# Optimization experiments

Measured on AMD Instinct MI355X. Metric: run time of the kernel, lower is better.

The kernel has to match this reference:

```python
import jax, jax.numpy as jnp
import numpy as np


def setup_inputs() -> dict:
    key = jax.random.key(0)
    ks = jax.random.split(key, 8)
    B, S, H, I = 2, 1025, 3200, 12800
    T = B * S
    # int8 tensors represented as int32, symmetric range [-128, 126]
    hidden_states = jax.random.randint(ks[0], (B, S, H), 0, 255, dtype=jnp.int32) - 127
    scale_in = (jax.random.uniform(ks[1], (T,)) * 0.02 + 1e-4).astype(jnp.float16)
    w1 = jax.random.randint(ks[2], (I, H), 0, 255, dtype=jnp.int32) - 127
    w1_scale = (jax.random.uniform(ks[3], (I,)) * 0.01 + 1e-4).astype(jnp.float32)
    b1 = (jax.random.normal(ks[4], (I,)) * 0.02).astype(jnp.float16)
    w2 = jax.random.randint(ks[5], (H, I), 0, 255, dtype=jnp.int32) - 127
    w2_scale = (jax.random.uniform(ks[6], (H,)) * 0.01 + 1e-4).astype(jnp.float32)
    b2 = (jax.random.normal(ks[7], (H,)) * 0.02).astype(jnp.float16)
    return {"hidden_states": hidden_states, "scale_in": scale_in,
            "w1": w1, "w1_scale": w1_scale, "b1": b1,
            "w2": w2, "w2_scale": w2_scale, "b2": b2}


def _w8a8_linear(x_int, scale_x, w_int, w_scale, bias):
    # int8 GEMM with int32 accumulation, dequant with per-token * per-channel scales
    acc = jnp.matmul(x_int, w_int.T)  # [T, out] int32
    out = acc.astype(jnp.float32) * scale_x[:, None].astype(jnp.float32) * w_scale[None, :]
    return (out + bias.astype(jnp.float32)).astype(jnp.float16)


def _gelu_and_quant(x_f16):
    # fused GELU + per-token dynamic symmetric int8 quantization
    g = jax.nn.gelu(x_f16.astype(jnp.float32), approximate=False)  # [T, I]
    amax = jnp.max(jnp.abs(g), axis=-1)                              # [T]
    scale_act = (amax / 127.0).astype(jnp.float16)
    s = jnp.maximum(scale_act.astype(jnp.float32), 1e-8)
    q = jnp.clip(jnp.round(g / s[:, None]), -128, 127).astype(jnp.int32)
    return q, scale_act


def reference(hidden_states, scale_in, w1, w1_scale, b1, w2, w2_scale, b2):
    B, S, H = hidden_states.shape
    x = hidden_states.reshape(-1, H)               # [T, H] int
    fc1_out = _w8a8_linear(x, scale_in, w1, w1_scale, b1)      # [T, I] fp16
    act_out, scale_act = _gelu_and_quant(fc1_out)              # int8-as-int32, [T] fp16
    fc2_out = _w8a8_linear(act_out, scale_act, w2, w2_scale, b2)  # [T, H] fp16
    return fc2_out
```

## Files before the change

### kernel.cpp

```cpp
#include <hip/hip_runtime.h>
#include <hip/hip_fp16.h>

typedef int v4i __attribute__((ext_vector_type(4)));

#define AS1C(p) ((const __attribute__((address_space(1))) void*)(p))
#define AS3(p)  ((__attribute__((address_space(3))) void*)(p))

__global__ void pack1(const int* __restrict__ a, const int* __restrict__ b,
                      signed char* __restrict__ pa, signed char* __restrict__ pb,
                      unsigned int* __restrict__ amax,
                      long long na, long long nb, int T) {
  const long long gid = blockIdx.x * (long long)blockDim.x + threadIdx.x;
  if (gid < T) amax[gid] = 0u;
  const long long n4a = na >> 2, n4b = nb >> 2;
  const long long tot = n4a + n4b;
  const long long stride = (long long)gridDim.x * blockDim.x;
  for (long long u = gid; u < tot; u += stride) {
    const int* src; signed char* dst; long long loc;
    if (u < n4a) { src = a; dst = pa; loc = u; }
    else         { src = b; dst = pb; loc = u - n4a; }
    const int4 v = *(const int4*)(src + (loc << 2));
    const unsigned out = (unsigned)(v.x & 0xff) | ((unsigned)(v.y & 0xff) << 8) |
                         ((unsigned)(v.z & 0xff) << 16) | ((unsigned)(v.w & 0xff) << 24);
    *(unsigned*)(dst + (loc << 2)) = out;
  }
}

__launch_bounds__(1024, 4)
__global__ void fc1_fused(const signed char* __restrict__ A, const signed char* __restrict__ Bw,
                          int M, int N, int K,
                          const float* __restrict__ scale_tok, const float* __restrict__ wsc,
                          const float* __restrict__ bias,
                          __half* __restrict__ gout, unsigned int* __restrict__ amax,
                          const int* __restrict__ w2src, signed char* __restrict__ w2dst,
                          long long n4w2, int npack, int gy) {
  __shared__ __align__(16) char smem[2][32768];
  const int bid = blockIdx.x;

  if (bid < npack) {
    const long long stride = (long long)npack * 1024;
    for (long long u = (long long)bid * 1024 + threadIdx.x; u < n4w2; u += stride) {
      const int4 v = *(const int4*)(w2src + (u << 2));
      const unsigned out = (unsigned)(v.x & 0xff) | ((unsigned)(v.y & 0xff) << 8) |
                           ((unsigned)(v.z & 0xff) << 16) | ((unsigned)(v.w & 0xff) << 24);
      *(unsigned*)(w2dst + (u << 2)) = out;
    }
    return;
  }

  const int tid = threadIdx.x;
  const int lane = tid & 63, wave = tid >> 6;
  const int wavem = wave >> 2, waven = wave & 3;
  const int lh = lane & 15, sseg = lane >> 4;

  int lid;
  {
    const int o = bid - npack;
    const int nwg = gridDim.x - npack;
    const int q = nwg >> 3, r = nwg & 7;
    const int x = o & 7, p = o >> 3;
    lid = (x < r ? x * (q + 1) : r * (q + 1) + (x - r) * q) + p;
  }
  const long long t0 = (long long)(lid % gy) * 256;
  const long long n0 = (long long)(lid / gy) * 256;
  const int nk = K >> 6;
  const long long Mm1 = M - 1, Nm1 = N - 1;

  const int lr4 = lane >> 2, slot = lane & 3;
  const int rloc = wave * 16 + lr4;
  const int gslot = (slot ^ ((rloc >> 1) & 3)) << 4;
  const signed char* sp0;
  const signed char* sp1;
  {
    long long gr = t0 + rloc; if (gr > Mm1) gr = Mm1;
    sp0 = A + gr * (long long)K + gslot;
    long long gn = n0 + rloc; if (gn > Nm1) gn = Nm1;
    sp1 = Bw + gn * (long long)K + gslot;
  }
  const int d0 = wave * 1024, d1 = 16384 + wave * 1024;

#define STAGE(bi) do { \
    __builtin_amdgcn_global_load_lds(AS1C(sp0), AS3(&smem[bi][d0]), 16, 0, 0); sp0 += 64; \
    __builtin_amdgcn_global_load_lds(AS1C(sp1), AS3(&smem[bi][d1]), 16, 0, 0); sp1 += 64; \
  } while (0)

  const int xs = ((sseg ^ ((lh >> 1) & 3)) << 4);
  const int offA = wavem * 4096 + lh * 64 + xs;
  const int offB = 16384 + waven * 4096 + lh * 64 + xs;

  v4i acc[4][4] = {};

  STAGE(0);
  __syncthreads();

  int cur = 0;
  for (int kt = 0; kt < nk; ++kt) {
    if (kt + 1 < nk) STAGE(cur ^ 1);
    const char* base = smem[cur];
    v4i af[4], bf[2];
#pragma unroll
    for (int mi = 0; mi < 4; ++mi) af[mi] = *(const v4i*)(base + offA + mi * 1024);
    bf[0] = *(const v4i*)(base + offB);
    bf[1] = *(const v4i*)(base + offB + 1024);
#pragma unroll
    for (int mi = 0; mi < 4; ++mi) {
      acc[mi][0] = __builtin_amdgcn_mfma_i32_16x16x64_i8(af[mi], bf[0], acc[mi][0], 0, 0, 0);
      acc[mi][1] = __builtin_amdgcn_mfma_i32_16x16x64_i8(af[mi], bf[1], acc[mi][1], 0, 0, 0);
    }
    bf[0] = *(const v4i*)(base + offB + 2048);
    bf[1] = *(const v4i*)(base + offB + 3072);
#pragma unroll
    for (int mi = 0; mi < 4; ++mi) {
      acc[mi][2] = __builtin_amdgcn_mfma_i32_16x16x64_i8(af[mi], bf[0], acc[mi][2], 0, 0, 0);
      acc[mi][3] = __builtin_amdgcn_mfma_i32_16x16x64_i8(af[mi], bf[1], acc[mi][3], 0, 0, 0);
    }
    __syncthreads();
    cur ^= 1;
  }
#undef STAGE

  long long cidx[4]; float w4[4], bi4[4]; bool cok[4];
#pragma unroll
  for (int ni = 0; ni < 4; ++ni) {
    cidx[ni] = n0 + waven * 64 + ni * 16 + lh;
    cok[ni] = cidx[ni] < N;
    w4[ni] = cok[ni] ? wsc[cidx[ni]] : 0.f;
    bi4[ni] = cok[ni] ? bias[cidx[ni]] : 0.f;
  }
#pragma unroll
  for (int mi = 0; mi < 4; ++mi) {
#pragma unroll
    for (int j = 0; j < 4; ++j) {
      const long long t = t0 + wavem * 64 + mi * 16 + (lane >> 4) * 4 + j;
      const bool valid = t < M;
      const float st = valid ? scale_tok[t] : 0.f;
      float rowmax = 0.f;
#pragma unroll
      for (int ni = 0; ni < 4; ++ni) {
        float v = (float)acc[mi][ni][j] * st * w4[ni] + bi4[ni];
        v = __half2float(__float2half(v));
        const float gl = 0.5f * v * (1.f + erff(v * 0.70710678118654752f));
        rowmax = fmaxf(rowmax, fabsf(gl));
        if (valid && cok[ni]) gout[t * (long long)N + cidx[ni]] = __float2half(gl);
      }
#pragma unroll
      for (int m = 1; m < 16; m <<= 1) rowmax = fmaxf(rowmax, __shfl_xor(rowmax, m));
      if (valid && lh == 0) atomicMax(&amax[t], __float_as_uint(rowmax));
    }
  }
}

__device__ __forceinline__ void stage_tile(const signed char* __restrict__ g, long long ld,
                                           long long rmax, long long r0, int k0,
                                           char* lds, int tid) {
  const int wave = tid >> 6, lane = tid & 63;
#pragma unroll
  for (int p = 0; p < 2; ++p) {
    const int chunk = wave * 2 + p;
    const int row = chunk * 16 + (lane >> 2);
    const int slot = lane & 3;
    const int gslot = slot ^ ((row >> 1) & 3);
    long long rg = r0 + row;
    if (rg > rmax) rg = rmax;
    const signed char* src = g + rg * ld + (long long)k0 + gslot * 16;
    char* dst = lds + chunk * 1024;
    __builtin_amdgcn_global_load_lds(AS1C(src), AS3(dst), 16, 0, 0);
  }
}

__launch_bounds__(256, 4)
__global__ void gemm_fc2(const signed char* __restrict__ A, const signed char* __restrict__ Bw,
                         int M, int N, int K,
                         const float* __restrict__ wsc, const float* __restrict__ bias,
                         unsigned int* __restrict__ amax, float* __restrict__ fout) {
  __shared__ __align__(16) char lds[2][2][128 * 64];
  const int tid = threadIdx.x;
  const int lane = tid & 63, wave = tid >> 6;
  const int wrow = (wave >> 1) * 64, wcol = (wave & 1) * 64;

  const int gy = gridDim.y;
  int lid;
  {
    const int o = blockIdx.y * gridDim.x + blockIdx.x;
    const int nwg = gridDim.x * gy;
    const int q = nwg >> 3, r = nwg & 7;
    const int x = o & 7, p = o >> 3;
    lid = (x < r ? x * (q + 1) : r * (q + 1) + (x - r) * q) + p;
  }
  const long long t0 = (long long)(lid % gy) * 128;
  const long long n0 = (long long)(lid / gy) * 128;

  v4i acc[4][4] = {};

  stage_tile(A, K, (long long)M - 1, t0, 0, lds[0][0], tid);
  stage_tile(Bw, K, (long long)N - 1, n0, 0, lds[0][1], tid);
  __syncthreads();

  const int nk = K >> 6;
  int cur = 0;
  const int srow = lane & 15, sseg = lane >> 4;
  for (int kt = 0; kt < nk; ++kt) {
    if (kt + 1 < nk) {
      stage_tile(A, K, (long long)M - 1, t0, (kt + 1) << 6, lds[cur ^ 1][0], tid);
      stage_tile(Bw, K, (long long)N - 1, n0, (kt + 1) << 6, lds[cur ^ 1][1], tid);
    }
    v4i af[4], bf[4];
#pragma unroll
    for (int mi = 0; mi < 4; ++mi) {
      const int r = wrow + mi * 16 + srow;
      const int sl = sseg ^ ((r >> 1) & 3);
      af[mi] = *(const v4i*)&lds[cur][0][r * 64 + sl * 16];
    }
#pragma unroll
    for (int ni = 0; ni < 4; ++ni) {
      const int r = wcol + ni * 16 + srow;
      const int sl = sseg ^ ((r >> 1) & 3);
      bf[ni] = *(const v4i*)&lds[cur][1][r * 64 + sl * 16];
    }
#pragma unroll
    for (int mi = 0; mi < 4; ++mi)
#pragma unroll
      for (int ni = 0; ni < 4; ++ni)
        acc[mi][ni] = __builtin_amdgcn_mfma_i32_16x16x64_i8(af[mi], bf[ni], acc[mi][ni], 0, 0, 0);
    __syncthreads();
    cur ^= 1;
  }

#pragma unroll
  for (int mi = 0; mi < 4; ++mi) {
#pragma unroll
    for (int j = 0; j < 4; ++j) {
      const long long t = t0 + wrow + mi * 16 + (lane >> 4) * 4 + j;
      if (t < M) {
        const float am = __uint_as_float(amax[t]);
        const float st = __half2float(__float2half(am * (1.f / 127.f)));
#pragma unroll
        for (int ni = 0; ni < 4; ++ni) {
          const long long c = n0 + wcol + ni * 16 + (lane & 15);
          const float v = (float)acc[mi][ni][j] * st * wsc[c] + bias[c];
          fout[t * (long long)N + c] = __half2float(__float2half(v));
        }
      }
    }
  }
}

__global__ void gelu_quant(const __half* __restrict__ g, const unsigned int* __restrict__ amax,
                           signed char* __restrict__ q, long long total, int I) {
  const long long nchunk = total >> 3;
  const long long stride = (long long)gridDim.x * blockDim.x;
  for (long long c = blockIdx.x * (long long)blockDim.x + threadIdx.x; c < nchunk; c += stride) {
    const long long base = c << 3;
    const int t = (int)(base / I);
    const float am = __uint_as_float(amax[t]);
    const float s = fmaxf(__half2float(__float2half(am * (1.f / 127.f))), 1e-8f);
    const float inv = 1.f / s;
    const int4 raw = *(const int4*)(g + base);
    const __half2* h2 = (const __half2*)&raw;
    union { signed char b[8]; int2 v; } u;
#pragma unroll
    for (int k = 0; k < 4; ++k) {
      const float2 f = __half22float2(h2[k]);
      const float q0 = fminf(fmaxf(rintf(f.x * inv), -128.f), 127.f);
      const float q1 = fminf(fmaxf(rintf(f.y * inv), -128.f), 127.f);
      u.b[k * 2]     = (signed char)(int)q0;
      u.b[k * 2 + 1] = (signed char)(int)q1;
    }
    *(int2*)(q + base) = u.v;
  }
}

extern "C" void kernel_launch(void* const* d_in, const int* in_sizes, int n_in,
                              void* d_out, int out_size, void* d_ws, size_t ws_size,
                              hipStream_t stream) {
  const int* hs = (const int*)d_in[0];
  const float* scale_in = (const float*)d_in[1];
  const int* w1 = (const int*)d_in[2];
  const float* w1s = (const float*)d_in[3];
  const float* b1 = (const float*)d_in[4];
  const int* w2 = (const int*)d_in[5];
  const float* w2s = (const float*)d_in[6];
  const float* b2 = (const float*)d_in[7];

  const int T = in_sizes[1];
  const int I = in_sizes[3];
  const int H = in_sizes[6];

  char* ws = (char*)d_ws;
  unsigned int* amax = (unsigned int*)ws;
  signed char* px  = (signed char*)(ws + 16384);
  signed char* pw1 = px + (size_t)T * H;
  signed char* pw2 = pw1 + (size_t)I * H;
  __half* gbuf = (__half*)(pw2 + (size_t)H * I);
  signed char* qbuf = (signed char*)(gbuf + (size_t)T * I);

  const long long nx = (long long)T * H, nw1 = (long long)I * H, nw2 = (long long)H * I;

  pack1<<<2048, 256, 0, stream>>>(hs, w1, px, pw1, amax, nx, nw1, T);

  const int NPACK = 62;
  const int gy1 = (T + 255) / 256;
  const int gemmBlocks = (I / 256) * gy1;
  fc1_fused<<<NPACK + gemmBlocks, 1024, 0, stream>>>(
      px, pw1, T, I, H, scale_in, w1s, b1, gbuf, amax,
      w2, pw2, nw2 >> 2, NPACK, gy1);

  gelu_quant<<<2048, 256, 0, stream>>>(gbuf, amax, qbuf, (long long)T * I, I);

  dim3 g2(H / 128, (T + 127) / 128);
  gemm_fc2<<<g2, 256, 0, stream>>>(qbuf, pw2, T, H, I, w2s, b2, amax, (float*)d_out);
}
```

Measured before the change: 335.0 us.

## Enlarge fc2 GEMM tile to 128x256 with 512 threads and precomputed load pointers

The fc2 int8 GEMM now uses 128x256 output tiles with 8 waves instead of 128x128 with 4 waves. A-tile reuse goes up and the grid shrinks. Global-to-LDS staging uses precomputed per-thread pointers that advance by 64 bytes per step instead of recomputing addresses each time. B fragments are loaded in two halves to cut register pressure, and per-column scale and bias are hoisted out of the epilogue. Since 3200 is not a multiple of 256, the last column tile is partial and needs bounds checks, which leaves some idle work and fewer blocks to spread across CUs.

Measured after the change: 885.2 us. 164% more time.

```diff
diff --git a/kernel.cpp b/kernel.cpp
--- a/kernel.cpp
+++ b/kernel.cpp
@@ -150,33 +150,16 @@
   }
 }
 
-__device__ __forceinline__ void stage_tile(const signed char* __restrict__ g, long long ld,
-                                           long long rmax, long long r0, int k0,
-                                           char* lds, int tid) {
-  const int wave = tid >> 6, lane = tid & 63;
-#pragma unroll
-  for (int p = 0; p < 2; ++p) {
-    const int chunk = wave * 2 + p;
-    const int row = chunk * 16 + (lane >> 2);
-    const int slot = lane & 3;
-    const int gslot = slot ^ ((row >> 1) & 3);
-    long long rg = r0 + row;
-    if (rg > rmax) rg = rmax;
-    const signed char* src = g + rg * ld + (long long)k0 + gslot * 16;
-    char* dst = lds + chunk * 1024;
-    __builtin_amdgcn_global_load_lds(AS1C(src), AS3(dst), 16, 0, 0);
-  }
-}
-
-__launch_bounds__(256, 4)
+__launch_bounds__(512, 6)
 __global__ void gemm_fc2(const signed char* __restrict__ A, const signed char* __restrict__ Bw,
                          int M, int N, int K,
                          const float* __restrict__ wsc, const float* __restrict__ bias,
                          unsigned int* __restrict__ amax, float* __restrict__ fout) {
-  __shared__ __align__(16) char lds[2][2][128 * 64];
+  __shared__ __align__(16) char smem[2][24576];
   const int tid = threadIdx.x;
   const int lane = tid & 63, wave = tid >> 6;
-  const int wrow = (wave >> 1) * 64, wcol = (wave & 1) * 64;
+  const int wavem = wave >> 2, waven = wave & 3;
+  const int lh = lane & 15, sseg = lane >> 4;
 
   const int gy = gridDim.y;
   int lid;
@@ -188,57 +171,88 @@
     lid = (x < r ? x * (q + 1) : r * (q + 1) + (x - r) * q) + p;
   }
   const long long t0 = (long long)(lid % gy) * 128;
-  const long long n0 = (long long)(lid / gy) * 128;
+  const long long n0 = (long long)(lid / gy) * 256;
+  const int nk = K >> 6;
+  const long long Mm1 = M - 1, Nm1 = N - 1;
+
+  const signed char* sp[3];
+  int dst[3];
+#pragma unroll
+  for (int i = 0; i < 3; ++i) {
+    const int c = wave * 3 + i;
+    const bool isA = c < 8;
+    const int lr = (isA ? c : c - 8) * 16 + (lane >> 2);
+    const int gslot = (((lane & 3) ^ ((lr >> 1) & 3)) << 4);
+    long long gr = isA ? (t0 + lr) : (n0 + lr);
+    const long long rmax = isA ? Mm1 : Nm1;
+    if (gr > rmax) gr = rmax;
+    sp[i] = (isA ? A : Bw) + gr * (long long)K + gslot;
+    dst[i] = c * 1024;
+  }
+
+#define STAGE(bi) do { \
+    _Pragma("unroll") \
+    for (int i = 0; i < 3; ++i) { \
+      __builtin_amdgcn_global_load_lds(AS1C(sp[i]), AS3(&smem[bi][dst[i]]), 16, 0, 0); \
+      sp[i] += 64; \
+    } \
+  } while (0)
+
+  const int xs = ((sseg ^ ((lh >> 1) & 3)) << 4);
+  const int offA = wavem * 4096 + lh * 64 + xs;
+  const int offB = 8192 + waven * 4096 + lh * 64 + xs;
 
   v4i acc[4][4] = {};
 
-  stage_tile(A, K, (long long)M - 1, t0, 0, lds[0][0], tid);
-  stage_tile(Bw, K, (long long)N - 1, n0, 0, lds[0][1], tid);
+  STAGE(0);
   __syncthreads();
 
-  const int nk = K >> 6;
   int cur = 0;
-  const int srow = lane & 15, sseg = lane >> 4;
   for (int kt = 0; kt < nk; ++kt) {
-    if (kt + 1 < nk) {
-      stage_tile(A, K, (long long)M - 1, t0, (kt + 1) << 6, lds[cur ^ 1][0], tid);
-      stage_tile(Bw, K, (long long)N - 1, n0, (kt + 1) << 6, lds[cur ^ 1][1], tid);
-    }
-    v4i af[4], bf[4];
+    if (kt + 1 < nk) STAGE(cur ^ 1);
+    const char* base = smem[cur];
+    v4i af[4], bf[2];
+#pragma unroll
+    for (int mi = 0; mi < 4; ++mi) af[mi] = *(const v4i*)(base + offA + mi * 1024);
+    bf[0] = *(const v4i*)(base + offB);
+    bf[1] = *(const v4i*)(base + offB + 1024);
 #pragma unroll
     for (int mi = 0; mi < 4; ++mi) {
-      const int r = wrow + mi * 16 + srow;
-      const int sl = sseg ^ ((r >> 1) & 3);
-      af[mi] = *(const v4i*)&lds[cur][0][r * 64 + sl * 16];
-    }
-#pragma unroll
-    for (int ni = 0; ni < 4; ++ni) {
-      const int r = wcol + ni * 16 + srow;
-      const int sl = sseg ^ ((r >> 1) & 3);
-      bf[ni] = *(const v4i*)&lds[cur][1][r * 64 + sl * 16];
-    }
-#pragma unroll
-    for (int mi = 0; mi < 4; ++mi)
-#pragma unroll
-      for (int ni = 0; ni < 4; ++ni)
-        acc[mi][ni] = __builtin_amdgcn_mfma_i32_16x16x64_i8(af[mi], bf[ni], acc[mi][ni], 0, 0, 0);
+      acc[mi][0] = __builtin_amdgcn_mfma_i32_16x16x64_i8(af[mi], bf[0], acc[mi][0], 0, 0, 0);
+      acc[mi][1] = __builtin_amdgcn_mfma_i32_16x16x64_i8(af[mi], bf[1], acc[mi][1], 0, 0, 0);
+    }
+    bf[0] = *(const v4i*)(base + offB + 2048);
+    bf[1] = *(const v4i*)(base + offB + 3072);
+#pragma unroll
+    for (int mi = 0; mi < 4; ++mi) {
+      acc[mi][2] = __builtin_amdgcn_mfma_i32_16x16x64_i8(af[mi], bf[0], acc[mi][2], 0, 0, 0);
+      acc[mi][3] = __builtin_amdgcn_mfma_i32_16x16x64_i8(af[mi], bf[1], acc[mi][3], 0, 0, 0);
+    }
     __syncthreads();
     cur ^= 1;
   }
-
+#undef STAGE
+
+  long long cidx[4]; float w4[4], bi4[4]; bool cok[4];
+#pragma unroll
+  for (int ni = 0; ni < 4; ++ni) {
+    cidx[ni] = n0 + waven * 64 + ni * 16 + lh;
+    cok[ni] = cidx[ni] < N;
+    w4[ni] = cok[ni] ? wsc[cidx[ni]] : 0.f;
+    bi4[ni] = cok[ni] ? bias[cidx[ni]] : 0.f;
+  }
 #pragma unroll
   for (int mi = 0; mi < 4; ++mi) {
 #pragma unroll
     for (int j = 0; j < 4; ++j) {
-      const long long t = t0 + wrow + mi * 16 + (lane >> 4) * 4 + j;
+      const long long t = t0 + wavem * 64 + mi * 16 + (lane >> 4) * 4 + j;
       if (t < M) {
         const float am = __uint_as_float(amax[t]);
         const float st = __half2float(__float2half(am * (1.f / 127.f)));
 #pragma unroll
         for (int ni = 0; ni < 4; ++ni) {
-          const long long c = n0 + wcol + ni * 16 + (lane & 15);
-          const float v = (float)acc[mi][ni][j] * st * wsc[c] + bias[c];
-          fout[t * (long long)N + c] = __half2float(__float2half(v));
+          const float v = (float)acc[mi][ni][j] * st * w4[ni] + bi4[ni];
+          if (cok[ni]) fout[t * (long long)N + cidx[ni]] = __half2float(__float2half(v));
         }
       }
     }
@@ -307,6 +321,6 @@
 
   gelu_quant<<<2048, 256, 0, stream>>>(gbuf, amax, qbuf, (long long)T * I, I);
 
-  dim3 g2(H / 128, (T + 127) / 128);
-  gemm_fc2<<<g2, 256, 0, stream>>>(qbuf, pw2, T, H, I, w2s, b2, amax, (float*)d_out);
-}
+  dim3 g2((H + 255) / 256, (T + 127) / 128);
+  gemm_fc2<<<g2, 512, 0, stream>>>(qbuf, pw2, T, H, I, w2s, b2, amax, (float*)d_out);
+}
```

## Split-K the FC2 GEMM in two and add a separate dequant reduce kernel

Applied to the files above, without the earlier changes.

Each FC2 output tile is now computed by two workgroups, each covering half of K. They write int32 partial sums into a scratch buffer that reuses the GELU fp16 buffer. A new reduce kernel adds the two partials and applies the per-token scale, per-channel scale and bias. The staging addresses are also precomputed and advanced by pointer increments, which removes per-iteration index math. The goal is more workgroups for better CU occupancy on a 25x17-tile grid, paid for by extra global traffic for the int32 partials and one more kernel launch.

After: 340.2 us. Within noise of the previous version (+1.5%).

```diff
diff --git a/kernel.cpp b/kernel.cpp
--- a/kernel.cpp
+++ b/kernel.cpp
@@ -150,73 +150,72 @@
   }
 }
 
-__device__ __forceinline__ void stage_tile(const signed char* __restrict__ g, long long ld,
-                                           long long rmax, long long r0, int k0,
-                                           char* lds, int tid) {
-  const int wave = tid >> 6, lane = tid & 63;
-#pragma unroll
-  for (int p = 0; p < 2; ++p) {
-    const int chunk = wave * 2 + p;
-    const int row = chunk * 16 + (lane >> 2);
-    const int slot = lane & 3;
-    const int gslot = slot ^ ((row >> 1) & 3);
-    long long rg = r0 + row;
-    if (rg > rmax) rg = rmax;
-    const signed char* src = g + rg * ld + (long long)k0 + gslot * 16;
-    char* dst = lds + chunk * 1024;
-    __builtin_amdgcn_global_load_lds(AS1C(src), AS3(dst), 16, 0, 0);
-  }
-}
-
 __launch_bounds__(256, 4)
-__global__ void gemm_fc2(const signed char* __restrict__ A, const signed char* __restrict__ Bw,
-                         int M, int N, int K,
-                         const float* __restrict__ wsc, const float* __restrict__ bias,
-                         unsigned int* __restrict__ amax, float* __restrict__ fout) {
+__global__ void gemm_fc2s(const signed char* __restrict__ A, const signed char* __restrict__ Bw,
+                          int M, int N, int K, int* __restrict__ pbuf) {
   __shared__ __align__(16) char lds[2][2][128 * 64];
   const int tid = threadIdx.x;
   const int lane = tid & 63, wave = tid >> 6;
   const int wrow = (wave >> 1) * 64, wcol = (wave & 1) * 64;
 
-  const int gy = gridDim.y;
+  const int z = blockIdx.x & 1;
+  const int o = blockIdx.x >> 1;
+  const int gy = (M + 127) >> 7;
+  const int nwg = gridDim.x >> 1;
   int lid;
   {
-    const int o = blockIdx.y * gridDim.x + blockIdx.x;
-    const int nwg = gridDim.x * gy;
     const int q = nwg >> 3, r = nwg & 7;
     const int x = o & 7, p = o >> 3;
     lid = (x < r ? x * (q + 1) : r * (q + 1) + (x - r) * q) + p;
   }
   const long long t0 = (long long)(lid % gy) * 128;
   const long long n0 = (long long)(lid / gy) * 128;
+  const int koff = z * (K >> 1);
+  const int nk = (K >> 1) >> 6;
+  const long long Mm1 = M - 1, Nm1 = N - 1;
+
+  const signed char* sp[4];
+  int dst[4];
+#pragma unroll
+  for (int i = 0; i < 4; ++i) {
+    const bool isA = i < 2;
+    const int c = wave * 2 + (i & 1);
+    const int lr = c * 16 + (lane >> 2);
+    const int gslot = (((lane & 3) ^ ((lr >> 1) & 3)) << 4);
+    long long gr = (isA ? t0 : n0) + lr;
+    const long long rmax = isA ? Mm1 : Nm1;
+    if (gr > rmax) gr = rmax;
+    sp[i] = (isA ? A : Bw) + gr * (long long)K + koff + gslot;
+    dst[i] = (isA ? 0 : 8192) + c * 1024;
+  }
+
+#define STAGE(bi) do { \
+    _Pragma("unroll") \
+    for (int i = 0; i < 4; ++i) { \
+      __builtin_amdgcn_global_load_lds(AS1C(sp[i]), AS3(&lds[bi][0][0] + dst[i]), 16, 0, 0); \
+      sp[i] += 64; \
+    } \
+  } while (0)
+
+  const int srow = lane & 15, sseg = lane >> 4;
+  const int xs = ((sseg ^ ((srow >> 1) & 3)) << 4);
+  const int offA = (wrow + srow) * 64 + xs;
+  const int offB = 8192 + (wcol + srow) * 64 + xs;
 
   v4i acc[4][4] = {};
 
-  stage_tile(A, K, (long long)M - 1, t0, 0, lds[0][0], tid);
-  stage_tile(Bw, K, (long long)N - 1, n0, 0, lds[0][1], tid);
+  STAGE(0);
   __syncthreads();
 
-  const int nk = K >> 6;
   int cur = 0;
-  const int srow = lane & 15, sseg = lane >> 4;
   for (int kt = 0; kt < nk; ++kt) {
-    if (kt + 1 < nk) {
-      stage_tile(A, K, (long long)M - 1, t0, (kt + 1) << 6, lds[cur ^ 1][0], tid);
-      stage_tile(Bw, K, (long long)N - 1, n0, (kt + 1) << 6, lds[cur ^ 1][1], tid);
-    }
+    if (kt + 1 < nk) STAGE(cur ^ 1);
+    const char* base = &lds[cur][0][0];
     v4i af[4], bf[4];
 #pragma unroll
-    for (int mi = 0; mi < 4; ++mi) {
-      const int r = wrow + mi * 16 + srow;
-      const int sl = sseg ^ ((r >> 1) & 3);
-      af[mi] = *(const v4i*)&lds[cur][0][r * 64 + sl * 16];
-    }
-#pragma unroll
-    for (int ni = 0; ni < 4; ++ni) {
-      const int r = wcol + ni * 16 + srow;
-      const int sl = sseg ^ ((r >> 1) & 3);
-      bf[ni] = *(const v4i*)&lds[cur][1][r * 64 + sl * 16];
-    }
+    for (int mi = 0; mi < 4; ++mi) af[mi] = *(const v4i*)(base + offA + mi * 1024);
+#pragma unroll
+    for (int ni = 0; ni < 4; ++ni) bf[ni] = *(const v4i*)(base + offB + ni * 1024);
 #pragma unroll
     for (int mi = 0; mi < 4; ++mi)
 #pragma unroll
@@ -225,23 +224,48 @@
     __syncthreads();
     cur ^= 1;
   }
-
+#undef STAGE
+
+  const long long zbase = (long long)z * M * N;
 #pragma unroll
   for (int mi = 0; mi < 4; ++mi) {
 #pragma unroll
     for (int j = 0; j < 4; ++j) {
       const long long t = t0 + wrow + mi * 16 + (lane >> 4) * 4 + j;
       if (t < M) {
-        const float am = __uint_as_float(amax[t]);
-        const float st = __half2float(__float2half(am * (1.f / 127.f)));
 #pragma unroll
         for (int ni = 0; ni < 4; ++ni) {
           const long long c = n0 + wcol + ni * 16 + (lane & 15);
-          const float v = (float)acc[mi][ni][j] * st * wsc[c] + bias[c];
-          fout[t * (long long)N + c] = __half2float(__float2half(v));
+          pbuf[zbase + t * (long long)N + c] = acc[mi][ni][j];
         }
       }
     }
+  }
+}
+
+__global__ void fc2_reduce(const int* __restrict__ pbuf, const unsigned int* __restrict__ amax,
+                           const float* __restrict__ wsc, const float* __restrict__ bias,
+                           float* __restrict__ out, int T_, int N_) {
+  const long long MN = (long long)T_ * N_;
+  const long long nchunk = MN >> 2;
+  const long long stride = (long long)gridDim.x * blockDim.x;
+  for (long long cchunk = blockIdx.x * (long long)blockDim.x + threadIdx.x;
+       cchunk < nchunk; cchunk += stride) {
+    const long long base = cchunk << 2;
+    const int t = (int)(base / N_);
+    const int n = (int)(base - (long long)t * N_);
+    const float am = __uint_as_float(amax[t]);
+    const float st = __half2float(__float2half(am * (1.f / 127.f)));
+    const int4 p0 = *(const int4*)(pbuf + base);
+    const int4 p1 = *(const int4*)(pbuf + MN + base);
+    const float4 w = *(const float4*)(wsc + n);
+    const float4 b = *(const float4*)(bias + n);
+    float4 o;
+    o.x = __half2float(__float2half((float)(p0.x + p1.x) * st * w.x + b.x));
+    o.y = __half2float(__float2half((float)(p0.y + p1.y) * st * w.y + b.y));
+    o.z = __half2float(__float2half((float)(p0.z + p1.z) * st * w.z + b.z));
+    o.w = __half2float(__float2half((float)(p0.w + p1.w) * st * w.w + b.w));
+    *(float4*)(out + base) = o;
   }
 }
 
@@ -293,6 +317,7 @@
   signed char* pw2 = pw1 + (size_t)I * H;
   __half* gbuf = (__half*)(pw2 + (size_t)H * I);
   signed char* qbuf = (signed char*)(gbuf + (size_t)T * I);
+  int* pbuf = (int*)gbuf;
 
   const long long nx = (long long)T * H, nw1 = (long long)I * H, nw2 = (long long)H * I;
 
@@ -307,6 +332,8 @@
 
   gelu_quant<<<2048, 256, 0, stream>>>(gbuf, amax, qbuf, (long long)T * I, I);
 
-  dim3 g2(H / 128, (T + 127) / 128);
-  gemm_fc2<<<g2, 256, 0, stream>>>(qbuf, pw2, T, H, I, w2s, b2, amax, (float*)d_out);
-}
+  const int tiles2 = (H / 128) * ((T + 127) / 128);
+  gemm_fc2s<<<tiles2 * 2, 256, 0, stream>>>(qbuf, pw2, T, H, I, pbuf);
+
+  fc2_reduce<<<2048, 256, 0, stream>>>(pbuf, amax, w2s, b2, (float*)d_out, T, H);
+}
```
